# Kernel optimization log

Measured on AMD Instinct MI355X. Metric: run time of the kernel, lower is better.

Reference implementation:

```python
import jax, jax.numpy as jnp
import numpy as np
from jax import lax

E = 256          # embed_dim
D = 2 * E        # d_model
V = 100000       # num_symbols (pad idx = V)
B = 2048         # query batch
NB = 30          # fixed neighbor window (hardcoded in source)
FEW = 3          # hardcoded support set size (view(3,1,2E))
STEPS = 4        # query encoder process steps
EPS = 1e-3       # LayerNormalization eps


def setup_inputs() -> dict:
    key = jax.random.key(0)
    ks = iter(jax.random.split(key, 48))
    def n(shape, s=0.05):
        return jax.random.normal(next(ks), shape, jnp.float32) * s
    inp = {}
    inp["query"] = n((B, D))
    inp["support"] = n((FEW, D))
    inp["query_left_connections"] = jax.random.randint(next(ks), (B, NB, 2), 0, V)
    inp["query_left_degrees"] = jax.random.randint(next(ks), (B,), 1, NB)
    inp["query_right_connections"] = jax.random.randint(next(ks), (B, NB, 2), 0, V)
    inp["query_right_degrees"] = jax.random.randint(next(ks), (B,), 1, NB)
    inp["support_left_connections"] = jax.random.randint(next(ks), (FEW, NB, 2), 0, V)
    inp["support_left_degrees"] = jax.random.randint(next(ks), (FEW,), 1, NB)
    inp["support_right_connections"] = jax.random.randint(next(ks), (FEW, NB, 2), 0, V)
    inp["support_right_degrees"] = jax.random.randint(next(ks), (FEW,), 1, NB)
    # parameters
    inp["emb"] = n((V + 1, E), 0.02).at[V].set(0.0)   # padding_idx row = 0
    inp["naW"] = n((E, D)); inp["naB"] = jnp.zeros((E,), jnp.float32)
    inp["nuW"] = n((1, E)); inp["nuB"] = jnp.zeros((1,), jnp.float32)
    inp["p1W"] = n((2 * D, D)); inp["p1b"] = jnp.zeros((2 * D,), jnp.float32)
    inp["p2W"] = n((D, 2 * D)); inp["p2b"] = jnp.zeros((D,), jnp.float32)
    inp["lnA"] = jnp.ones((D,), jnp.float32); inp["lnB"] = jnp.zeros((D,), jnp.float32)
    inp["encWih"] = n((4 * D, D)); inp["encWhh"] = n((4 * D, D))
    inp["encBih"] = jnp.zeros((4 * D,), jnp.float32); inp["encBhh"] = jnp.zeros((4 * D,), jnp.float32)
    inp["decWih"] = n((4 * D, D)); inp["decWhh"] = n((4 * D, D))
    inp["decBih"] = jnp.zeros((4 * D,), jnp.float32); inp["decBhh"] = jnp.zeros((4 * D,), jnp.float32)
    inp["saW"] = n((E, D)); inp["saB"] = jnp.zeros((E,), jnp.float32)
    inp["suW"] = n((1, E)); inp["suB"] = jnp.zeros((1,), jnp.float32)
    inp["qWih"] = n((8 * D, D)); inp["qWhh"] = n((8 * D, 2 * D))
    inp["qBih"] = jnp.zeros((8 * D,), jnp.float32); inp["qBhh"] = jnp.zeros((8 * D,), jnp.float32)
    return inp


def _lstm_cell(x, h, c, Wih, Whh, bih, bhh):
    g = x @ Wih.T + bih + h @ Whh.T + bhh
    i, f, gg, o = jnp.split(g, 4, axis=-1)
    c = jax.nn.sigmoid(f) * c + jax.nn.sigmoid(i) * jnp.tanh(gg)
    h = jax.nn.sigmoid(o) * jnp.tanh(c)
    return h, c


def _layer_norm(z, a, b):
    # torch.std is unbiased (ddof=1); eps is added to sigma, not variance
    mu = jnp.mean(z, axis=-1, keepdims=True)
    sigma = jnp.std(z, axis=-1, keepdims=True, ddof=1)
    return (z - mu) / (sigma + EPS) * a + b


def _neighbor_encoder(conn, emb, naW, naB, nuW, nuB):
    rel = emb[conn[..., 0]]                 # [N,30,E] gather
    ent = emb[conn[..., 1]]                 # [N,30,E] gather
    cat = jnp.concatenate([rel, ent], -1)   # [N,30,2E]
    out = jnp.tanh(cat @ naW.T + naB)       # [N,30,E]
    att = jax.nn.softmax(out @ nuW.T + nuB, axis=1)  # softmax over 30 neighbors
    agg = jnp.einsum('nk,nke->ne', att[..., 0], ent)  # weighted bmm reduce
    return jnp.tanh(agg)


def _support_encoder(x, p1W, p1b, p2W, p2b, lnA, lnB):
    h = jax.nn.relu(x @ p1W.T + p1b)
    o = h @ p2W.T + p2b
    return _layer_norm(o + x, lnA, lnB)


def reference(query, support,
              query_left_connections, query_left_degrees,
              query_right_connections, query_right_degrees,
              support_left_connections, support_left_degrees,
              support_right_connections, support_right_degrees,
              emb, naW, naB, nuW, nuB, p1W, p1b, p2W, p2b, lnA, lnB,
              encWih, encWhh, encBih, encBhh, decWih, decWhh, decBih, decBhh,
              saW, saB, suW, suB, qWih, qWhh, qBih, qBhh):
    ne = lambda c: _neighbor_encoder(c, emb, naW, naB, nuW, nuB)
    query_neighbor = jnp.concatenate([ne(query_left_connections), ne(query_right_connections)], -1)    # [B,2E]
    support_neighbor = jnp.concatenate([ne(support_left_connections), ne(support_right_connections)], -1)  # [3,2E]

    support_g = _support_encoder(support_neighbor, p1W, p1b, p2W, p2b, lnA, lnB)  # [3,D]
    query_g = _support_encoder(query_neighbor, p1W, p1b, p2W, p2b, lnA, lnB)      # [B,D]

    # set autoencoder: LSTM over the 3 support vectors (seq=3, batch=1)
    support_g_0 = support_g.reshape(FEW, 1, D)
    def enc_step(carry, x):
        h, c = carry
        h, c = _lstm_cell(x, h, c, encWih, encWhh, encBih, encBhh)
        return (h, c), h
    z = jnp.zeros((1, D), support_g.dtype)
    (h_f, c_f), enc_out = lax.scan(enc_step, (z, z), support_g_0)  # enc_out [3,1,D]

    # decoder: feed back its own output 3 times, init from encoder state
    h_d, c_d = h_f, c_f
    x = enc_out[-1]
    outs = []
    for _ in range(FEW):
        h_d, c_d = _lstm_cell(x, h_d, c_d, decWih, decWhh, decBih, decBhh)
        outs.append(h_d)
        x = h_d
    decoder_set = jnp.stack(outs)  # [3,1,D]
    ae_loss = jnp.mean((support_g_0 - lax.stop_gradient(decoder_set)) ** 2)

    sge = support_g_0.reshape(FEW, D) + enc_out.reshape(FEW, D)
    satt = jnp.tanh(sge @ saW.T + saB)                       # [3,E]
    aw = jax.nn.softmax(satt @ suW.T + suB, axis=1)          # softmax over dim of size 1 -> ones (faithful)
    support_g_encoder = (sge.T @ aw).T.reshape(1, D)         # [1,D]

    # query encoder: LSTMCell(D -> 2D) process loop
    h_r = jnp.zeros((query_g.shape[0], 2 * D), query_g.dtype)
    c = jnp.zeros_like(h_r)
    for _ in range(STEPS):
        h_r_, c = _lstm_cell(query_g, h_r, c, qWih, qWhh, qBih, qBhh)
        h = query_g + h_r_[:, :D]
        attn = jax.nn.softmax(h @ support_g_encoder.T, axis=1)  # [B,1] -> ones (faithful)
        r = attn @ support_g_encoder                            # [B,D]
        h_r = jnp.concatenate([h, r], axis=1)
    query_f = h

    matching_scores = (query_f @ support_g_encoder.T)[:, 0]    # [B]
    return (matching_scores, ae_loss, support_g_encoder, query_g)
```

## Files before the change

kernel.cpp:

```cpp
#include <hip/hip_runtime.h>
#include <hip/hip_bf16.h>

typedef unsigned short u16;
typedef __attribute__((ext_vector_type(8))) short bf16x8;
typedef __attribute__((ext_vector_type(4))) float f32x4;
#define MFMA16(a,b,c) __builtin_amdgcn_mfma_f32_16x16x32_bf16(a,b,c,0,0,0)
#define VPAD 100000

__device__ __forceinline__ float sigf(float x){ return 1.0f/(1.0f + __expf(-x)); }
__device__ __forceinline__ float ftanh(float x){
    float ax = fabsf(x);
    float e = __expf(-2.f*ax);
    float r = (1.f - e) / (1.f + e);
    return copysignf(r, x);
}
__device__ __forceinline__ u16 f2b(float f){
    unsigned u = __float_as_uint(f);
    u += 0x7fffu + ((u >> 16) & 1u);
    return (u16)(u >> 16);
}
__device__ __forceinline__ unsigned int pk2(float x, float y){
    return ((unsigned)f2b(y) << 16) | (unsigned)f2b(x);
}
__device__ __forceinline__ float b2f(u16 u){
    return __uint_as_float(((unsigned int)u) << 16);
}
__device__ __forceinline__ bf16x8 packA(float4 x, float4 y){
    union { bf16x8 v; uint4 u; } r;
    r.u.x = pk2(x.x,x.y); r.u.y = pk2(x.z,x.w);
    r.u.z = pk2(y.x,y.y); r.u.w = pk2(y.z,y.w);
    return r.v;
}

__global__ __launch_bounds__(256) void prep_kernel(
    const float* __restrict__ emb, const float* __restrict__ p1W,
    const float* __restrict__ p2W, const float* __restrict__ naW,
    const float* __restrict__ qWih, const float* __restrict__ qWhh,
    const float* __restrict__ qBih, const float* __restrict__ qBhh,
    u16* __restrict__ embbf, u16* __restrict__ p1Wb, u16* __restrict__ p2Wb,
    u16* __restrict__ nawf, u16* __restrict__ WihS, u16* __restrict__ WhhS,
    float* __restrict__ bc, int useBf)
{
    const long gid = (long)blockIdx.x * 256 + threadIdx.x;
    const long E0 = 6400064;
    const long E1 = E0 + 131072;
    const long E2 = E1 + 131072;
    const long E3 = E2 + 131072;
    const long E4 = E3 + 131072;
    const long E5 = E4 + 16384;
    const long E6 = E5 + 2048;
    if (gid < E0){
        if (!useBf) return;
        float4 v = reinterpret_cast<const float4*>(emb)[gid];
        uint2 s; s.x = pk2(v.x,v.y); s.y = pk2(v.z,v.w);
        reinterpret_cast<uint2*>(embbf)[gid] = s;
    } else if (gid < E1){
        long i = gid - E0;
        float4 v = reinterpret_cast<const float4*>(p1W)[i];
        uint2 s; s.x = pk2(v.x,v.y); s.y = pk2(v.z,v.w);
        reinterpret_cast<uint2*>(p1Wb)[i] = s;
    } else if (gid < E2){
        long i = gid - E1;
        float4 v = reinterpret_cast<const float4*>(p2W)[i];
        uint2 s; s.x = pk2(v.x,v.y); s.y = pk2(v.z,v.w);
        reinterpret_cast<uint2*>(p2Wb)[i] = s;
    } else if (gid < E3){
        long j = gid - E2;
        int n = (int)(j >> 6), c8 = (int)(j & 63);
        int srow = (n & 3) * 1024 + (n >> 2);
        const float* sp = qWih + (size_t)srow * 512 + c8 * 8;
        float4 a = *reinterpret_cast<const float4*>(sp);
        float4 b = *reinterpret_cast<const float4*>(sp + 4);
        uint4 o; o.x = pk2(a.x,a.y); o.y = pk2(a.z,a.w);
        o.z = pk2(b.x,b.y); o.w = pk2(b.z,b.w);
        *reinterpret_cast<uint4*>(WihS + (size_t)n*512 + c8*8) = o;
    } else if (gid < E4){
        long j = gid - E3;
        int n = (int)(j >> 6), c8 = (int)(j & 63);
        int srow = (n & 3) * 1024 + (n >> 2);
        const float* sp = qWhh + (size_t)srow * 1024 + c8 * 8;
        float4 a = *reinterpret_cast<const float4*>(sp);
        float4 b = *reinterpret_cast<const float4*>(sp + 4);
        uint4 o; o.x = pk2(a.x,a.y); o.y = pk2(a.z,a.w);
        o.z = pk2(b.x,b.y); o.w = pk2(b.z,b.w);
        *reinterpret_cast<uint4*>(WhhS + (size_t)n*512 + c8*8) = o;
    } else if (gid < E5){
        long j = gid - E4;
        int f = (int)(j >> 6), lane = (int)(j & 63);
        int ks = f >> 4, ig = f & 15;
        int col = lane & 15, quad = lane >> 4;
        int n = ig*16 + col;
        int k0 = ks*32 + quad*8;
        const float* sp = naW + (size_t)n*512 + k0;
        float4 a = *reinterpret_cast<const float4*>(sp);
        float4 b = *reinterpret_cast<const float4*>(sp + 4);
        uint4 o; o.x = pk2(a.x,a.y); o.y = pk2(a.z,a.w);
        o.z = pk2(b.x,b.y); o.w = pk2(b.z,b.w);
        *reinterpret_cast<uint4*>(nawf + j*8) = o;
    } else if (gid < E6){
        int n = (int)(gid - E5);
        int row = (n & 3) * 1024 + (n >> 2);
        bc[n] = qBih[row] + qBhh[row];
    }
}

__global__ __launch_bounds__(256) void neighbor_v3(
    const int* __restrict__ qL, const int* __restrict__ qR,
    const int* __restrict__ sL, const int* __restrict__ sR,
    const float* __restrict__ embf, const u16* __restrict__ embb, int useBf,
    const u16* __restrict__ nawf,
    const float* __restrict__ naB, const float* __restrict__ nuW,
    const float* __restrict__ nuB,
    float* __restrict__ out, u16* __restrict__ out_bf)
{
    __shared__ int relid[2][32];
    __shared__ int entid[2][32];
    __shared__ float logit[2][32];
    __shared__ float att[2][32];

    const int t = threadIdx.x;
    const int row = blockIdx.x;
    if (t < 128){
        int s = t >> 6, j = t & 63;
        int k = j >> 1, which = j & 1;
        const int* conn;
        if (row < 2048) conn = (s ? qR : qL) + (size_t)row * 60;
        else            conn = (s ? sR : sL) + (size_t)(row - 2048) * 60;
        int id = (k < 30) ? conn[k*2 + which] : VPAD;
        if (which) entid[s][k] = id; else relid[s][k] = id;
    }
    if (t >= 128 && t < 192){ int s = (t-128) >> 5; logit[s][(t-128)&31] = 0.f; }
    __syncthreads();

    const int w = t >> 6, lane = t & 63;
    const int col = lane & 15, quad = lane >> 4;

    int ridv[4], eidv[4];
    #pragma unroll
    for (int u = 0; u < 4; u++){
        int s = u >> 1, mt = u & 1;
        int kn = mt*16 + col;
        ridv[u] = relid[s][kn];
        eidv[u] = entid[s][kn];
    }

    f32x4 acc[4][4] = {};

    if (useBf){
        const u16* baseR[4];
        const u16* baseE[4];
        #pragma unroll
        for (int u = 0; u < 4; u++){
            baseR[u] = embb + (size_t)ridv[u]*256 + quad*8;
            baseE[u] = embb + (size_t)eidv[u]*256 + quad*8;
        }
        #pragma unroll
        for (int ks = 0; ks < 16; ks++){
            const int off = (ks & 7) * 32;
            bf16x8 a[4], b[4];
            #pragma unroll
            for (int u = 0; u < 4; u++)
                a[u] = *reinterpret_cast<const bf16x8*>((ks < 8 ? baseR[u] : baseE[u]) + off);
            #pragma unroll
            for (int i = 0; i < 4; i++)
                b[i] = *reinterpret_cast<const bf16x8*>(nawf + ((size_t)(ks*16 + w*4 + i)*64 + lane)*8);
            #pragma unroll
            for (int i = 0; i < 4; i++)
                #pragma unroll
                for (int u = 0; u < 4; u++)
                    acc[u][i] = MFMA16(a[u], b[i], acc[u][i]);
        }
    } else {
        const float* baseR[4];
        const float* baseE[4];
        #pragma unroll
        for (int u = 0; u < 4; u++){
            baseR[u] = embf + (size_t)ridv[u]*256 + quad*8;
            baseE[u] = embf + (size_t)eidv[u]*256 + quad*8;
        }
        #pragma unroll
        for (int ks = 0; ks < 16; ks++){
            const int off = (ks & 7) * 32;
            bf16x8 a[4], b[4];
            #pragma unroll
            for (int u = 0; u < 4; u++){
                const float* p = (ks < 8 ? baseR[u] : baseE[u]) + off;
                float4 x = *reinterpret_cast<const float4*>(p);
                float4 y = *reinterpret_cast<const float4*>(p + 4);
                a[u] = packA(x, y);
            }
            #pragma unroll
            for (int i = 0; i < 4; i++)
                b[i] = *reinterpret_cast<const bf16x8*>(nawf + ((size_t)(ks*16 + w*4 + i)*64 + lane)*8);
            #pragma unroll
            for (int i = 0; i < 4; i++)
                #pragma unroll
                for (int u = 0; u < 4; u++)
                    acc[u][i] = MFMA16(a[u], b[i], acc[u][i]);
        }
    }

    float nu[4], nbv[4];
    #pragma unroll
    for (int i = 0; i < 4; i++){
        int n = (w*4 + i)*16 + col;
        nu[i] = nuW[n]; nbv[i] = naB[n];
    }
    #pragma unroll
    for (int u = 0; u < 4; u++){
        int s = u >> 1, mt = u & 1;
        #pragma unroll
        for (int r = 0; r < 4; r++){
            int m = mt*16 + quad*4 + r;
            float v = 0.f;
            #pragma unroll
            for (int i = 0; i < 4; i++)
                v += ftanh(acc[u][i][r] + nbv[i]) * nu[i];
            v += __shfl_xor(v, 1); v += __shfl_xor(v, 2);
            v += __shfl_xor(v, 4); v += __shfl_xor(v, 8);
            if (col == 0 && m < 30) atomicAdd(&logit[s][m], v);
        }
    }
    __syncthreads();

    if (t < 2){
        const int s = t;
        const float nub = nuB[0];
        float mx = -1e30f;
        float lg[30];
        #pragma unroll
        for (int k = 0; k < 30; k++){
            float L = logit[s][k] + nub;
            lg[k] = L; mx = fmaxf(mx, L);
        }
        float sm = 0.f;
        #pragma unroll
        for (int k = 0; k < 30; k++){ float e = __expf(lg[k]-mx); att[s][k] = e; sm += e; }
        float inv = 1.f / sm;
        #pragma unroll
        for (int k = 0; k < 30; k++) att[s][k] *= inv;
    }
    __syncthreads();

    const int e = t;
    #pragma unroll
    for (int s = 0; s < 2; s++){
        float agg = 0.f;
        #pragma unroll
        for (int k = 0; k < 30; k++){
            int id = entid[s][k];
            float ev = useBf ? b2f(embb[(size_t)id*256 + e])
                             : embf[(size_t)id*256 + e];
            agg += att[s][k] * ev;
        }
        float r = ftanh(agg);
        size_t oi = (size_t)row*512 + s*256 + e;
        out[oi] = r;
        out_bf[oi] = f2b(r);
    }
}

__global__ __launch_bounds__(256) void gemm128(
    const u16* __restrict__ A, int lda,
    const u16* __restrict__ B, int ldb,
    const float* __restrict__ bias,
    const float* __restrict__ addD, int ldd,
    float* __restrict__ Cf, u16* __restrict__ Cbf, int ldc,
    int K, int relu)
{
    __shared__ __align__(16) u16 As[128][72];
    __shared__ __align__(16) u16 Bs[128][72];
    const int t = threadIdx.x;
    const int m0 = blockIdx.y * 128, n0 = blockIdx.x * 128;
    const int w = t >> 6, lane = t & 63;
    const int col = lane & 15, quad = lane >> 4;
    const int wm = (w & 1) * 64, wn = (w >> 1) * 64;

    const int srow = t >> 1, sseg = t & 1;
    const u16* Ap = A + (size_t)(m0 + srow) * lda + sseg * 32;
    const u16* Bp = B + (size_t)(n0 + srow) * ldb + sseg * 32;

    f32x4 acc[4][4] = {};

    const int KC = K >> 6;
    for (int kc = 0; kc < KC; kc++){
        uint4 av[4], bv[4];
        #pragma unroll
        for (int j = 0; j < 4; j++){
            av[j] = *reinterpret_cast<const uint4*>(Ap + kc*64 + j*8);
            bv[j] = *reinterpret_cast<const uint4*>(Bp + kc*64 + j*8);
        }
        __syncthreads();
        #pragma unroll
        for (int j = 0; j < 4; j++){
            *reinterpret_cast<uint4*>(&As[srow][sseg*32 + j*8]) = av[j];
            *reinterpret_cast<uint4*>(&Bs[srow][sseg*32 + j*8]) = bv[j];
        }
        __syncthreads();
        #pragma unroll
        for (int ks = 0; ks < 2; ks++){
            const int k0 = ks*32 + quad*8;
            bf16x8 af[4], bf[4];
            #pragma unroll
            for (int i = 0; i < 4; i++) af[i] = *reinterpret_cast<const bf16x8*>(&As[wm + i*16 + col][k0]);
            #pragma unroll
            for (int j = 0; j < 4; j++) bf[j] = *reinterpret_cast<const bf16x8*>(&Bs[wn + j*16 + col][k0]);
            #pragma unroll
            for (int i = 0; i < 4; i++)
                #pragma unroll
                for (int j = 0; j < 4; j++)
                    acc[i][j] = MFMA16(af[i], bf[j], acc[i][j]);
        }
    }

    #pragma unroll
    for (int j = 0; j < 4; j++){
        int n = n0 + wn + j*16 + col;
        float bj = bias[n];
        #pragma unroll
        for (int i = 0; i < 4; i++){
            #pragma unroll
            for (int r = 0; r < 4; r++){
                int m = m0 + wm + i*16 + quad*4 + r;
                float v = acc[i][j][r] + bj;
                if (addD) v += addD[(size_t)m*ldd + n];
                if (relu) v = fmaxf(v, 0.f);
                if (Cf)  Cf[(size_t)m*ldc + n] = v;
                if (Cbf) Cbf[(size_t)m*ldc + n] = f2b(v);
            }
        }
    }
}

__global__ __launch_bounds__(256) void ln_kernel(
    const float* __restrict__ Z, const float* __restrict__ X, int N, int nquery,
    const float* __restrict__ lnA, const float* __restrict__ lnB,
    float* __restrict__ Y, u16* __restrict__ Ybf, float* __restrict__ Ycopy)
{
    const int wv = threadIdx.x >> 6, lane = threadIdx.x & 63;
    const int row = blockIdx.x * 4 + wv;
    if (row >= N) return;
    const float* z = Z + (size_t)row * 512;
    const float* x = X + (size_t)row * 512;
    float v[8];
    float s = 0.f, ss = 0.f;
    {
        float4 z0 = *reinterpret_cast<const float4*>(z + lane*8);
        float4 z1 = *reinterpret_cast<const float4*>(z + lane*8 + 4);
        float4 x0 = *reinterpret_cast<const float4*>(x + lane*8);
        float4 x1 = *reinterpret_cast<const float4*>(x + lane*8 + 4);
        v[0]=z0.x+x0.x; v[1]=z0.y+x0.y; v[2]=z0.z+x0.z; v[3]=z0.w+x0.w;
        v[4]=z1.x+x1.x; v[5]=z1.y+x1.y; v[6]=z1.z+x1.z; v[7]=z1.w+x1.w;
    }
    #pragma unroll
    for (int u = 0; u < 8; u++){ s += v[u]; ss += v[u]*v[u]; }
    #pragma unroll
    for (int d = 1; d < 64; d <<= 1){
        s  += __shfl_xor(s, d);
        ss += __shfl_xor(ss, d);
    }
    float mu  = s * (1.f/512.f);
    float var = (ss - 512.f*mu*mu) * (1.f/511.f);
    float sd  = sqrtf(fmaxf(var, 0.f));
    float inv = 1.f / (sd + 1e-3f);
    float o[8];
    #pragma unroll
    for (int u = 0; u < 8; u++){
        int e = lane*8 + u;
        o[u] = (v[u] - mu) * inv * lnA[e] + lnB[e];
    }
    float* yr = Y + (size_t)row*512 + lane*8;
    *reinterpret_cast<float4*>(yr)     = make_float4(o[0],o[1],o[2],o[3]);
    *reinterpret_cast<float4*>(yr + 4) = make_float4(o[4],o[5],o[6],o[7]);
    if (row < nquery){
        uint4 p;
        p.x = pk2(o[0],o[1]); p.y = pk2(o[2],o[3]);
        p.z = pk2(o[4],o[5]); p.w = pk2(o[6],o[7]);
        *reinterpret_cast<uint4*>(Ybf + (size_t)row*512 + lane*8) = p;
        float* cr = Ycopy + (size_t)row*512 + lane*8;
        *reinterpret_cast<float4*>(cr)     = make_float4(o[0],o[1],o[2],o[3]);
        *reinterpret_cast<float4*>(cr + 4) = make_float4(o[4],o[5],o[6],o[7]);
    }
}

__global__ __launch_bounds__(256) void lstm_small(
    const float* __restrict__ x, const float* __restrict__ hin,
    float* __restrict__ c,
    const float* __restrict__ Wih, const float* __restrict__ Whh,
    const float* __restrict__ bih, const float* __restrict__ bhh,
    float* __restrict__ hout)
{
    __shared__ float xs[512], hs[512];
    __shared__ float gbuf[4][4];
    const int t = threadIdx.x;
    for (int i = t; i < 512; i += 256){ xs[i] = x[i]; hs[i] = hin[i]; }
    __syncthreads();

    const int wd = t >> 6;
    const int lane = t & 63;
    const int g = lane >> 4, p = lane & 15;
    const int d = blockIdx.x*4 + wd;
    const int j = g*512 + d;
    const float4* wi = reinterpret_cast<const float4*>(Wih + (size_t)j*512) + p*8;
    const float4* wh = reinterpret_cast<const float4*>(Whh + (size_t)j*512) + p*8;
    float acc = 0.f;
    #pragma unroll
    for (int q = 0; q < 8; q++){
        float4 wv = wi[q];
        const int kb = p*32 + q*4;
        acc += xs[kb]*wv.x + xs[kb+1]*wv.y + xs[kb+2]*wv.z + xs[kb+3]*wv.w;
        float4 vv = wh[q];
        acc += hs[kb]*vv.x + hs[kb+1]*vv.y + hs[kb+2]*vv.z + hs[kb+3]*vv.w;
    }
    acc += __shfl_xor(acc, 1); acc += __shfl_xor(acc, 2);
    acc += __shfl_xor(acc, 4); acc += __shfl_xor(acc, 8);
    if (p == 0) gbuf[wd][g] = acc + bih[j] + bhh[j];
    __syncthreads();
    if (t < 4){
        int dd = blockIdx.x*4 + t;
        float iv = gbuf[t][0], fv = gbuf[t][1], gv = gbuf[t][2], ov = gbuf[t][3];
        float cn = sigf(fv)*c[dd] + sigf(iv)*ftanh(gv);
        float hn = sigf(ov)*ftanh(cn);
        c[dd] = cn; hout[dd] = hn;
    }
}

__global__ __launch_bounds__(256) void finalize_kernel(
    const float* __restrict__ sg, const float* __restrict__ enc,
    const float* __restrict__ dec, float* __restrict__ sgeenc,
    float* __restrict__ outp)
{
    __shared__ float red[4];
    const int t = threadIdx.x;
    float s = 0.f;
    for (int i = t; i < 1536; i += 256){ float d = sg[i] - dec[i]; s += d*d; }
    s += __shfl_xor(s,1); s += __shfl_xor(s,2); s += __shfl_xor(s,4);
    s += __shfl_xor(s,8); s += __shfl_xor(s,16); s += __shfl_xor(s,32);
    if ((t & 63) == 0) red[t>>6] = s;
    __syncthreads();
    if (t == 0){
        float tot = (red[0]+red[1]+red[2]+red[3]) * (1.f/1536.f);
        outp[2048] = tot;
    }
    for (int d = t; d < 512; d += 256){
        float v = sg[d] + enc[d] + sg[512+d] + enc[512+d] + sg[1024+d] + enc[1024+d];
        sgeenc[d] = v;
        outp[2049 + d] = v;
    }
}

__global__ __launch_bounds__(256) void wvec_kernel(
    const float* __restrict__ qWhh, const float* __restrict__ sge,
    float* __restrict__ wvec)
{
    __shared__ float ss[512];
    const int t = threadIdx.x;
    for (int i = t; i < 512; i += 256) ss[i] = sge[i];
    __syncthreads();
    const int n = blockIdx.x * 256 + t;
    const int row = (n & 3) * 1024 + (n >> 2);
    const float4* w = reinterpret_cast<const float4*>(qWhh + (size_t)row*1024 + 512);
    float acc = 0.f;
    for (int kc = 0; kc < 128; kc++){
        float4 wv = w[kc];
        const int kb = kc*4;
        acc += ss[kb]*wv.x + ss[kb+1]*wv.y + ss[kb+2]*wv.z + ss[kb+3]*wv.w;
    }
    wvec[n] = acc;
}

__global__ __launch_bounds__(256) void gate_kernel(
    const float* __restrict__ G, const float* __restrict__ qg,
    float* __restrict__ c, u16* __restrict__ h_bf)
{
    const int idx = blockIdx.x * 256 + threadIdx.x;
    const int b = idx >> 9, d = idx & 511;
    float4 g4 = *reinterpret_cast<const float4*>(G + (size_t)b*2048 + d*4);
    float cn = sigf(g4.y)*c[idx] + sigf(g4.x)*ftanh(g4.z);
    float hn = qg[idx] + sigf(g4.w)*ftanh(cn);
    c[idx] = cn; h_bf[idx] = f2b(hn);
}

__global__ __launch_bounds__(256) void scores_kernel(
    const u16* __restrict__ h, const float* __restrict__ sge,
    float* __restrict__ out)
{
    const int wave = threadIdx.x >> 6, lane = threadIdx.x & 63;
    const int row = blockIdx.x * 4 + wave;
    const u16* hr = h + (size_t)row * 512;
    float s = 0.f;
    for (int i = lane; i < 512; i += 64) s += b2f(hr[i]) * sge[i];
    s += __shfl_xor(s,1); s += __shfl_xor(s,2); s += __shfl_xor(s,4);
    s += __shfl_xor(s,8); s += __shfl_xor(s,16); s += __shfl_xor(s,32);
    if (lane == 0) out[row] = s;
}

extern "C" void kernel_launch(void* const* d_in, const int* in_sizes, int n_in,
                              void* d_out, int out_size, void* d_ws, size_t ws_size,
                              hipStream_t stream)
{
    (void)in_sizes; (void)n_in; (void)out_size;

    const int* qlc = (const int*)d_in[2];
    const int* qrc = (const int*)d_in[4];
    const int* slc = (const int*)d_in[6];
    const int* src = (const int*)d_in[8];
    const float* emb = (const float*)d_in[10];
    const float* naW = (const float*)d_in[11];
    const float* naB = (const float*)d_in[12];
    const float* nuW = (const float*)d_in[13];
    const float* nuB = (const float*)d_in[14];
    const float* p1W = (const float*)d_in[15], *p1b = (const float*)d_in[16];
    const float* p2W = (const float*)d_in[17], *p2b = (const float*)d_in[18];
    const float* lnA = (const float*)d_in[19], *lnB = (const float*)d_in[20];
    const float* eWih = (const float*)d_in[21], *eWhh = (const float*)d_in[22];
    const float* eBih = (const float*)d_in[23], *eBhh = (const float*)d_in[24];
    const float* dWih = (const float*)d_in[25], *dWhh = (const float*)d_in[26];
    const float* dBih = (const float*)d_in[27], *dBhh = (const float*)d_in[28];
    const float* qWih = (const float*)d_in[33], *qWhh = (const float*)d_in[34];
    const float* qBih = (const float*)d_in[35], *qBhh = (const float*)d_in[36];
    float* out = (float*)d_out;

    float* w = (float*)d_ws;
    size_t off = 0;
    auto alloc = [&](size_t nelem){ float* p = w + off; off += nelem; return p; };
    float* qn    = alloc(2176ull*512);
    float* qg    = alloc(2176ull*512);
    float* enc   = alloc(1536);
    float* dec   = alloc(1536);
    float* zc    = alloc(1024);
    float* sgee  = alloc(512);
    float* wv    = alloc(2048);
    float* bc    = alloc(2048);
    float* nawfF = alloc(65536);
    float* base  = alloc(2048ull*2048);
    float* G     = alloc(2048ull*2048);
    float* cb    = alloc(2048ull*512);
    float* hbfF  = alloc(524288);
    float* p1WbF = alloc(262144);
    float* p2WbF = alloc(262144);
    float* WihSF = alloc(524288);
    float* WhhSF = alloc(524288);
    size_t needNoEmb = off;
    float* embbF = alloc(12800128);
    size_t needEmb = off;
    int useBf = (ws_size >= needEmb * sizeof(float)) ? 1 : 0;
    (void)needNoEmb;

    u16* nawf   = (u16*)nawfF;
    u16* p1Wb   = (u16*)p1WbF;
    u16* p2Wb   = (u16*)p2WbF;
    u16* WihSel = (u16*)WihSF;
    u16* WhhSel = (u16*)WhhSF;
    u16* h_bf   = (u16*)hbfF;
    u16* embbf  = (u16*)embbF;
    float* Zq   = base;
    u16* qn_bf  = (u16*)(base + 2097152);
    u16* Hq_bf  = (u16*)G;
    u16* qg_bf  = (u16*)(G + 2097152);
    float* sg   = qg + 2048ull*512;
    float* zbuf = zc;
    float* cst  = zc + 512;

    hipMemsetAsync(zc, 0, 1024*sizeof(float), stream);
    hipMemsetAsync(cb, 0, 2048ull*512*sizeof(float), stream);

    prep_kernel<<<27121, 256, 0, stream>>>(emb, p1W, p2W, naW, qWih, qWhh, qBih, qBhh,
                                           embbf, p1Wb, p2Wb, nawf, WihSel, WhhSel,
                                           bc, useBf);

    neighbor_v3<<<2051, 256, 0, stream>>>(qlc, qrc, slc, src, emb, embbf, useBf,
                                          nawf, naB, nuW, nuB, qn, qn_bf);

    gemm128<<<dim3(8,17), 256, 0, stream>>>(qn_bf, 512, p1Wb, 512, p1b, nullptr, 0,
                                            nullptr, Hq_bf, 1024, 512, 1);
    gemm128<<<dim3(4,17), 256, 0, stream>>>(Hq_bf, 1024, p2Wb, 1024, p2b, nullptr, 0,
                                            Zq, nullptr, 512, 1024, 0);
    ln_kernel<<<513, 256, 0, stream>>>(Zq, qn, 2051, 2048, lnA, lnB, qg, qg_bf, out + 2561);

    lstm_small<<<128, 256, 0, stream>>>(sg,        zbuf,      cst, eWih, eWhh, eBih, eBhh, enc);
    lstm_small<<<128, 256, 0, stream>>>(sg + 512,  enc,       cst, eWih, eWhh, eBih, eBhh, enc + 512);
    lstm_small<<<128, 256, 0, stream>>>(sg + 1024, enc + 512, cst, eWih, eWhh, eBih, eBhh, enc + 1024);
    lstm_small<<<128, 256, 0, stream>>>(enc + 1024, enc + 1024, cst, dWih, dWhh, dBih, dBhh, dec);
    lstm_small<<<128, 256, 0, stream>>>(dec,        dec,        cst, dWih, dWhh, dBih, dBhh, dec + 512);
    lstm_small<<<128, 256, 0, stream>>>(dec + 512,  dec + 512,  cst, dWih, dWhh, dBih, dBhh, dec + 1024);

    finalize_kernel<<<1, 256, 0, stream>>>(sg, enc, dec, sgee, out);
    wvec_kernel<<<8, 256, 0, stream>>>(qWhh, sgee, wv);

    gemm128<<<dim3(16,16), 256, 0, stream>>>(qg_bf, 512, WihSel, 512, bc, nullptr, 0,
                                             base, nullptr, 2048, 512, 0);
    gate_kernel<<<4096, 256, 0, stream>>>(base, qg, cb, h_bf);
    for (int s = 0; s < 3; s++){
        gemm128<<<dim3(16,16), 256, 0, stream>>>(h_bf, 512, WhhSel, 512, wv, base, 2048,
                                                 G, nullptr, 2048, 512, 0);
        gate_kernel<<<4096, 256, 0, stream>>>(G, qg, cb, h_bf);
    }

    scores_kernel<<<512, 256, 0, stream>>>(h_bf, sgee, out);
}
```

Measured before the change: 718.3 us.

## Drop full embedding bf16 conversion; gather fp32 rows into LDS; narrow GEMM tiles

Removes the prep pass that converted the whole 100k×256 embedding table to bf16 every call. The neighbor kernel now gathers only the needed fp32 rows with coalesced loads, converts them to bf16 and stages them in a 32 KB shared-memory fragment layout before the MFMAs. The GEMM tile shrinks from 128x128 to 128x64 and the grids double, giving more blocks for occupancy. The cost is extra LDS use and syncs in the neighbor kernel, and the smaller GEMM tiles reuse data less.

```diff
diff --git a/kernel.cpp b/kernel.cpp
--- a/kernel.cpp
+++ b/kernel.cpp
@@ -25,67 +25,56 @@
 __device__ __forceinline__ float b2f(u16 u){
     return __uint_as_float(((unsigned int)u) << 16);
 }
-__device__ __forceinline__ bf16x8 packA(float4 x, float4 y){
-    union { bf16x8 v; uint4 u; } r;
-    r.u.x = pk2(x.x,x.y); r.u.y = pk2(x.z,x.w);
-    r.u.z = pk2(y.x,y.y); r.u.w = pk2(y.z,y.w);
-    return r.v;
+__device__ __forceinline__ uint4 pk8(float4 x, float4 y){
+    uint4 o;
+    o.x = pk2(x.x,x.y); o.y = pk2(x.z,x.w);
+    o.z = pk2(y.x,y.y); o.w = pk2(y.z,y.w);
+    return o;
 }
 
 __global__ __launch_bounds__(256) void prep_kernel(
-    const float* __restrict__ emb, const float* __restrict__ p1W,
-    const float* __restrict__ p2W, const float* __restrict__ naW,
+    const float* __restrict__ p1W, const float* __restrict__ p2W,
+    const float* __restrict__ naW,
     const float* __restrict__ qWih, const float* __restrict__ qWhh,
     const float* __restrict__ qBih, const float* __restrict__ qBhh,
-    u16* __restrict__ embbf, u16* __restrict__ p1Wb, u16* __restrict__ p2Wb,
+    u16* __restrict__ p1Wb, u16* __restrict__ p2Wb,
     u16* __restrict__ nawf, u16* __restrict__ WihS, u16* __restrict__ WhhS,
-    float* __restrict__ bc, int useBf)
+    float* __restrict__ bc)
 {
     const long gid = (long)blockIdx.x * 256 + threadIdx.x;
-    const long E0 = 6400064;
+    const long E0 = 131072;
     const long E1 = E0 + 131072;
     const long E2 = E1 + 131072;
     const long E3 = E2 + 131072;
-    const long E4 = E3 + 131072;
-    const long E5 = E4 + 16384;
-    const long E6 = E5 + 2048;
+    const long E4 = E3 + 16384;
+    const long E5 = E4 + 2048;
     if (gid < E0){
-        if (!useBf) return;
-        float4 v = reinterpret_cast<const float4*>(emb)[gid];
+        float4 v = reinterpret_cast<const float4*>(p1W)[gid];
         uint2 s; s.x = pk2(v.x,v.y); s.y = pk2(v.z,v.w);
-        reinterpret_cast<uint2*>(embbf)[gid] = s;
+        reinterpret_cast<uint2*>(p1Wb)[gid] = s;
     } else if (gid < E1){
         long i = gid - E0;
-        float4 v = reinterpret_cast<const float4*>(p1W)[i];
-        uint2 s; s.x = pk2(v.x,v.y); s.y = pk2(v.z,v.w);
-        reinterpret_cast<uint2*>(p1Wb)[i] = s;
-    } else if (gid < E2){
-        long i = gid - E1;
         float4 v = reinterpret_cast<const float4*>(p2W)[i];
         uint2 s; s.x = pk2(v.x,v.y); s.y = pk2(v.z,v.w);
         reinterpret_cast<uint2*>(p2Wb)[i] = s;
-    } else if (gid < E3){
-        long j = gid - E2;
+    } else if (gid < E2){
+        long j = gid - E1;
         int n = (int)(j >> 6), c8 = (int)(j & 63);
         int srow = (n & 3) * 1024 + (n >> 2);
         const float* sp = qWih + (size_t)srow * 512 + c8 * 8;
         float4 a = *reinterpret_cast<const float4*>(sp);
         float4 b = *reinterpret_cast<const float4*>(sp + 4);
-        uint4 o; o.x = pk2(a.x,a.y); o.y = pk2(a.z,a.w);
-        o.z = pk2(b.x,b.y); o.w = pk2(b.z,b.w);
-        *reinterpret_cast<uint4*>(WihS + (size_t)n*512 + c8*8) = o;
-    } else if (gid < E4){
-        long j = gid - E3;
+        *reinterpret_cast<uint4*>(WihS + (size_t)n*512 + c8*8) = pk8(a,b);
+    } else if (gid < E3){
+        long j = gid - E2;
         int n = (int)(j >> 6), c8 = (int)(j & 63);
         int srow = (n & 3) * 1024 + (n >> 2);
         const float* sp = qWhh + (size_t)srow * 1024 + c8 * 8;
         float4 a = *reinterpret_cast<const float4*>(sp);
         float4 b = *reinterpret_cast<const float4*>(sp + 4);
-        uint4 o; o.x = pk2(a.x,a.y); o.y = pk2(a.z,a.w);
-        o.z = pk2(b.x,b.y); o.w = pk2(b.z,b.w);
-        *reinterpret_cast<uint4*>(WhhS + (size_t)n*512 + c8*8) = o;
-    } else if (gid < E5){
-        long j = gid - E4;
+        *reinterpret_cast<uint4*>(WhhS + (size_t)n*512 + c8*8) = pk8(a,b);
+    } else if (gid < E4){
+        long j = gid - E3;
         int f = (int)(j >> 6), lane = (int)(j & 63);
         int ks = f >> 4, ig = f & 15;
         int col = lane & 15, quad = lane >> 4;
@@ -94,25 +83,24 @@
         const float* sp = naW + (size_t)n*512 + k0;
         float4 a = *reinterpret_cast<const float4*>(sp);
         float4 b = *reinterpret_cast<const float4*>(sp + 4);
-        uint4 o; o.x = pk2(a.x,a.y); o.y = pk2(a.z,a.w);
-        o.z = pk2(b.x,b.y); o.w = pk2(b.z,b.w);
-        *reinterpret_cast<uint4*>(nawf + j*8) = o;
-    } else if (gid < E6){
-        int n = (int)(gid - E5);
+        *reinterpret_cast<uint4*>(nawf + j*8) = pk8(a,b);
+    } else if (gid < E5){
+        int n = (int)(gid - E4);
         int row = (n & 3) * 1024 + (n >> 2);
         bc[n] = qBih[row] + qBhh[row];
     }
 }
 
-__global__ __launch_bounds__(256) void neighbor_v3(
+__global__ __launch_bounds__(256) void neighbor_v4(
     const int* __restrict__ qL, const int* __restrict__ qR,
     const int* __restrict__ sL, const int* __restrict__ sR,
-    const float* __restrict__ embf, const u16* __restrict__ embb, int useBf,
+    const float* __restrict__ emb,
     const u16* __restrict__ nawf,
     const float* __restrict__ naB, const float* __restrict__ nuW,
     const float* __restrict__ nuB,
     float* __restrict__ out, u16* __restrict__ out_bf)
 {
+    __shared__ __align__(16) u16 frg[32*512];
     __shared__ int relid[2][32];
     __shared__ int entid[2][32];
     __shared__ float logit[2][32];
@@ -135,32 +123,42 @@
     const int w = t >> 6, lane = t & 63;
     const int col = lane & 15, quad = lane >> 4;
 
-    int ridv[4], eidv[4];
-    #pragma unroll
-    for (int u = 0; u < 4; u++){
-        int s = u >> 1, mt = u & 1;
-        int kn = mt*16 + col;
-        ridv[u] = relid[s][kn];
-        eidv[u] = entid[s][kn];
+    int gc[8], gk[8], gs[8];
+    #pragma unroll
+    for (int i = 0; i < 8; i++){
+        int idx = i*256 + t;
+        gc[i] = idx & 31;
+        gk[i] = (idx >> 5) & 31;
+        gs[i] = idx >> 10;
     }
 
     f32x4 acc[4][4] = {};
 
-    if (useBf){
-        const u16* baseR[4];
-        const u16* baseE[4];
-        #pragma unroll
-        for (int u = 0; u < 4; u++){
-            baseR[u] = embb + (size_t)ridv[u]*256 + quad*8;
-            baseE[u] = embb + (size_t)eidv[u]*256 + quad*8;
-        }
-        #pragma unroll
-        for (int ks = 0; ks < 16; ks++){
-            const int off = (ks & 7) * 32;
+    #pragma unroll
+    for (int p = 0; p < 2; p++){
+        #pragma unroll
+        for (int i = 0; i < 8; i++){
+            int s = gs[i], k = gk[i], c = gc[i];
+            int e0 = c*8;
+            int id = p ? entid[s][k] : relid[s][k];
+            const float* ptr = emb + (size_t)id*256 + e0;
+            float4 x = *reinterpret_cast<const float4*>(ptr);
+            float4 y = *reinterpret_cast<const float4*>(ptr + 4);
+            int ksl = e0 >> 5, q = (e0 >> 3) & 3;
+            int mt = k >> 4, cl = k & 15;
+            int ln = q*16 + cl;
+            u16* dst = frg + ((((s*2 + mt)*8 + ksl)*64) + ln)*8;
+            *reinterpret_cast<uint4*>(dst) = pk8(x, y);
+        }
+        __syncthreads();
+
+        #pragma unroll
+        for (int ksl = 0; ksl < 8; ksl++){
             bf16x8 a[4], b[4];
             #pragma unroll
             for (int u = 0; u < 4; u++)
-                a[u] = *reinterpret_cast<const bf16x8*>((ks < 8 ? baseR[u] : baseE[u]) + off);
+                a[u] = *reinterpret_cast<const bf16x8*>(frg + (((u*8 + ksl)*64) + lane)*8);
+            const int ks = p*8 + ksl;
             #pragma unroll
             for (int i = 0; i < 4; i++)
                 b[i] = *reinterpret_cast<const bf16x8*>(nawf + ((size_t)(ks*16 + w*4 + i)*64 + lane)*8);
@@ -170,34 +168,7 @@
                 for (int u = 0; u < 4; u++)
                     acc[u][i] = MFMA16(a[u], b[i], acc[u][i]);
         }
-    } else {
-        const float* baseR[4];
-        const float* baseE[4];
-        #pragma unroll
-        for (int u = 0; u < 4; u++){
-            baseR[u] = embf + (size_t)ridv[u]*256 + quad*8;
-            baseE[u] = embf + (size_t)eidv[u]*256 + quad*8;
-        }
-        #pragma unroll
-        for (int ks = 0; ks < 16; ks++){
-            const int off = (ks & 7) * 32;
-            bf16x8 a[4], b[4];
-            #pragma unroll
-            for (int u = 0; u < 4; u++){
-                const float* p = (ks < 8 ? baseR[u] : baseE[u]) + off;
-                float4 x = *reinterpret_cast<const float4*>(p);
-                float4 y = *reinterpret_cast<const float4*>(p + 4);
-                a[u] = packA(x, y);
-            }
-            #pragma unroll
-            for (int i = 0; i < 4; i++)
-                b[i] = *reinterpret_cast<const bf16x8*>(nawf + ((size_t)(ks*16 + w*4 + i)*64 + lane)*8);
-            #pragma unroll
-            for (int i = 0; i < 4; i++)
-                #pragma unroll
-                for (int u = 0; u < 4; u++)
-                    acc[u][i] = MFMA16(a[u], b[i], acc[u][i]);
-        }
+        __syncthreads();
     }
 
     float nu[4], nbv[4];
@@ -249,9 +220,7 @@
         #pragma unroll
         for (int k = 0; k < 30; k++){
             int id = entid[s][k];
-            float ev = useBf ? b2f(embb[(size_t)id*256 + e])
-                             : embf[(size_t)id*256 + e];
-            agg += att[s][k] * ev;
+            agg += att[s][k] * emb[(size_t)id*256 + e];
         }
         float r = ftanh(agg);
         size_t oi = (size_t)row*512 + s*256 + e;
@@ -260,7 +229,7 @@
     }
 }
 
-__global__ __launch_bounds__(256) void gemm128(
+__global__ __launch_bounds__(256) void gemm_tn(
     const u16* __restrict__ A, int lda,
     const u16* __restrict__ B, int ldb,
     const float* __restrict__ bias,
@@ -269,52 +238,60 @@
     int K, int relu)
 {
     __shared__ __align__(16) u16 As[128][72];
-    __shared__ __align__(16) u16 Bs[128][72];
+    __shared__ __align__(16) u16 Bs[64][72];
     const int t = threadIdx.x;
-    const int m0 = blockIdx.y * 128, n0 = blockIdx.x * 128;
+    const int m0 = blockIdx.y * 128, n0 = blockIdx.x * 64;
     const int w = t >> 6, lane = t & 63;
     const int col = lane & 15, quad = lane >> 4;
-    const int wm = (w & 1) * 64, wn = (w >> 1) * 64;
-
-    const int srow = t >> 1, sseg = t & 1;
-    const u16* Ap = A + (size_t)(m0 + srow) * lda + sseg * 32;
-    const u16* Bp = B + (size_t)(n0 + srow) * ldb + sseg * 32;
-
-    f32x4 acc[4][4] = {};
+    const int wm = (w & 1) * 64, wn = (w >> 1) * 32;
+
+    int arow[4], aseg[4], brow[2], bseg[2];
+    #pragma unroll
+    for (int i = 0; i < 4; i++){
+        int idx = i*256 + t; arow[i] = idx >> 3; aseg[i] = (idx & 7) * 8;
+    }
+    #pragma unroll
+    for (int i = 0; i < 2; i++){
+        int idx = i*256 + t; brow[i] = idx >> 3; bseg[i] = (idx & 7) * 8;
+    }
+
+    f32x4 acc[4][2] = {};
 
     const int KC = K >> 6;
     for (int kc = 0; kc < KC; kc++){
-        uint4 av[4], bv[4];
-        #pragma unroll
-        for (int j = 0; j < 4; j++){
-            av[j] = *reinterpret_cast<const uint4*>(Ap + kc*64 + j*8);
-            bv[j] = *reinterpret_cast<const uint4*>(Bp + kc*64 + j*8);
-        }
+        uint4 av[4], bv[2];
+        #pragma unroll
+        for (int i = 0; i < 4; i++)
+            av[i] = *reinterpret_cast<const uint4*>(A + (size_t)(m0 + arow[i])*lda + kc*64 + aseg[i]);
+        #pragma unroll
+        for (int i = 0; i < 2; i++)
+            bv[i] = *reinterpret_cast<const uint4*>(B + (size_t)(n0 + brow[i])*ldb + kc*64 + bseg[i]);
         __syncthreads();
         #pragma unroll
-        for (int j = 0; j < 4; j++){
-            *reinterpret_cast<uint4*>(&As[srow][sseg*32 + j*8]) = av[j];
-            *reinterpret_cast<uint4*>(&Bs[srow][sseg*32 + j*8]) = bv[j];
-        }
+        for (int i = 0; i < 4; i++)
+            *reinterpret_cast<uint4*>(&As[arow[i]][aseg[i]]) = av[i];
+        #pragma unroll
+        for (int i = 0; i < 2; i++)
+            *reinterpret_cast<uint4*>(&Bs[brow[i]][bseg[i]]) = bv[i];
         __syncthreads();
         #pragma unroll
         for (int ks = 0; ks < 2; ks++){
             const int k0 = ks*32 + quad*8;
-            bf16x8 af[4], bf[4];
+            bf16x8 af[4], bf[2];
             #pragma unroll
             for (int i = 0; i < 4; i++) af[i] = *reinterpret_cast<const bf16x8*>(&As[wm + i*16 + col][k0]);
             #pragma unroll
-            for (int j = 0; j < 4; j++) bf[j] = *reinterpret_cast<const bf16x8*>(&Bs[wn + j*16 + col][k0]);
+            for (int j = 0; j < 2; j++) bf[j] = *reinterpret_cast<const bf16x8*>(&Bs[wn + j*16 + col][k0]);
             #pragma unroll
             for (int i = 0; i < 4; i++)
                 #pragma unroll
-                for (int j = 0; j < 4; j++)
+                for (int j = 0; j < 2; j++)
                     acc[i][j] = MFMA16(af[i], bf[j], acc[i][j]);
         }
     }
 
     #pragma unroll
-    for (int j = 0; j < 4; j++){
+    for (int j = 0; j < 2; j++){
         int n = n0 + wn + j*16 + col;
         float bj = bias[n];
         #pragma unroll
@@ -499,7 +476,7 @@
                               void* d_out, int out_size, void* d_ws, size_t ws_size,
                               hipStream_t stream)
 {
-    (void)in_sizes; (void)n_in; (void)out_size;
+    (void)in_sizes; (void)n_in; (void)out_size; (void)ws_size;
 
     const int* qlc = (const int*)d_in[2];
     const int* qrc = (const int*)d_in[4];
@@ -541,11 +518,6 @@
     float* p2WbF = alloc(262144);
     float* WihSF = alloc(524288);
     float* WhhSF = alloc(524288);
-    size_t needNoEmb = off;
-    float* embbF = alloc(12800128);
-    size_t needEmb = off;
-    int useBf = (ws_size >= needEmb * sizeof(float)) ? 1 : 0;
-    (void)needNoEmb;
 
     u16* nawf   = (u16*)nawfF;
     u16* p1Wb   = (u16*)p1WbF;
@@ -553,7 +525,6 @@
     u16* WihSel = (u16*)WihSF;
     u16* WhhSel = (u16*)WhhSF;
     u16* h_bf   = (u16*)hbfF;
-    u16* embbf  = (u16*)embbF;
     float* Zq   = base;
     u16* qn_bf  = (u16*)(base + 2097152);
     u16* Hq_bf  = (u16*)G;
@@ -565,16 +536,15 @@
     hipMemsetAsync(zc, 0, 1024*sizeof(float), stream);
     hipMemsetAsync(cb, 0, 2048ull*512*sizeof(float), stream);
 
-    prep_kernel<<<27121, 256, 0, stream>>>(emb, p1W, p2W, naW, qWih, qWhh, qBih, qBhh,
-                                           embbf, p1Wb, p2Wb, nawf, WihSel, WhhSel,
-                                           bc, useBf);
-
-    neighbor_v3<<<2051, 256, 0, stream>>>(qlc, qrc, slc, src, emb, embbf, useBf,
+    prep_kernel<<<2120, 256, 0, stream>>>(p1W, p2W, naW, qWih, qWhh, qBih, qBhh,
+                                          p1Wb, p2Wb, nawf, WihSel, WhhSel, bc);
+
+    neighbor_v4<<<2051, 256, 0, stream>>>(qlc, qrc, slc, src, emb,
                                           nawf, naB, nuW, nuB, qn, qn_bf);
 
-    gemm128<<<dim3(8,17), 256, 0, stream>>>(qn_bf, 512, p1Wb, 512, p1b, nullptr, 0,
-                                            nullptr, Hq_bf, 1024, 512, 1);
-    gemm128<<<dim3(4,17), 256, 0, stream>>>(Hq_bf, 1024, p2Wb, 1024, p2b, nullptr, 0,
+    gemm_tn<<<dim3(16,17), 256, 0, stream>>>(qn_bf, 512, p1Wb, 512, p1b, nullptr, 0,
+                                             nullptr, Hq_bf, 1024, 512, 1);
+    gemm_tn<<<dim3(8,17), 256, 0, stream>>>(Hq_bf, 1024, p2Wb, 1024, p2b, nullptr, 0,
                                             Zq, nullptr, 512, 1024, 0);
     ln_kernel<<<513, 256, 0, stream>>>(Zq, qn, 2051, 2048, lnA, lnB, qg, qg_bf, out + 2561);
 
@@ -588,11 +558,11 @@
     finalize_kernel<<<1, 256, 0, stream>>>(sg, enc, dec, sgee, out);
     wvec_kernel<<<8, 256, 0, stream>>>(qWhh, sgee, wv);
 
-    gemm128<<<dim3(16,16), 256, 0, stream>>>(qg_bf, 512, WihSel, 512, bc, nullptr, 0,
+    gemm_tn<<<dim3(32,16), 256, 0, stream>>>(qg_bf, 512, WihSel, 512, bc, nullptr, 0,
                                              base, nullptr, 2048, 512, 0);
     gate_kernel<<<4096, 256, 0, stream>>>(base, qg, cb, h_bf);
     for (int s = 0; s < 3; s++){
-        gemm128<<<dim3(16,16), 256, 0, stream>>>(h_bf, 512, WhhSel, 512, wv, base, 2048,
+        gemm_tn<<<dim3(32,16), 256, 0, stream>>>(h_bf, 512, WhhSel, 512, wv, base, 2048,
                                                  G, nullptr, 2048, 512, 0);
         gate_kernel<<<4096, 256, 0, stream>>>(G, qg, cb, h_bf);
     }
```

Result: faster. 633.9 us (-11.8%).
